# Kernel tuning notes

Hardware: AMD Instinct MI355X
Metric: run time of the kernel (lower is better)

The kernel has to match this reference:

```python
import jax, jax.numpy as jnp
import numpy as np

N, B, EMBED, ACT, DETER, STOCH, HID = 50, 256, 1536, 64, 2048, 64, 1024
EPS = 1e-3
MIN_STD, MAX_STD = 0.1, 2.0


def _p(key, shape, scale=0.02):
    return scale * jax.random.normal(key, shape, dtype=jnp.float32)


def setup_inputs() -> dict:
    key = jax.random.key(0)
    ks = jax.random.split(key, 20)
    inp = {
        "embed": jax.random.normal(ks[0], (N, B, EMBED), dtype=jnp.float32),
        "action": jax.random.normal(ks[1], (N, B, ACT), dtype=jnp.float32),
        "reset": jnp.zeros((N, B), dtype=bool),
        "h0": jnp.zeros((B, DETER), dtype=jnp.float32),
        "z0": jnp.zeros((B, STOCH), dtype=jnp.float32),
        "noises": jax.random.normal(ks[2], (N, B, STOCH), dtype=jnp.float32),
        # params
        "z_w": _p(ks[3], (STOCH, HID)), "z_b": jnp.zeros((HID,), jnp.float32),
        "a_w": _p(ks[4], (ACT, HID)),
        "in_g": jnp.ones((HID,), jnp.float32), "in_b": jnp.zeros((HID,), jnp.float32),
        "gru_wi": _p(ks[5], (HID, 3 * DETER)), "gru_wh": _p(ks[6], (DETER, 3 * DETER)),
        "gru_bi": jnp.zeros((3 * DETER,), jnp.float32), "gru_bh": jnp.zeros((3 * DETER,), jnp.float32),
        "ph_w": _p(ks[7], (DETER, HID)), "ph_b": jnp.zeros((HID,), jnp.float32),
        "pe_w": _p(ks[8], (EMBED, HID)),
        "pon_g": jnp.ones((HID,), jnp.float32), "pon_b": jnp.zeros((HID,), jnp.float32),
        "pom_w": _p(ks[9], (HID, 2 * STOCH)), "pom_b": jnp.zeros((2 * STOCH,), jnp.float32),
        "prh_w": _p(ks[10], (DETER, HID)), "prh_b": jnp.zeros((HID,), jnp.float32),
        "prn_g": jnp.ones((HID,), jnp.float32), "prn_b": jnp.zeros((HID,), jnp.float32),
        "prm_w": _p(ks[11], (HID, 2 * STOCH)), "prm_b": jnp.zeros((2 * STOCH,), jnp.float32),
    }
    return inp


def _ln(x, g, b):
    m = x.mean(-1, keepdims=True)
    v = ((x - m) ** 2).mean(-1, keepdims=True)
    return (x - m) * jax.lax.rsqrt(v + EPS) * g + b


def _rssm(embed, action, reset, h0, z0, noises,
          z_w, z_b, a_w, in_g, in_b, gru_wi, gru_wh, gru_bi, gru_bh,
          ph_w, ph_b, pe_w, pon_g, pon_b, pom_w, pom_b,
          prh_w, prh_b, prn_g, prn_b, prm_w, prm_b):
    mask = (~reset).astype(jnp.float32)[..., None]  # [n,b,1]

    def step(carry, xs):
        h, z = carry
        e, a, m, nz = xs
        h = h * m
        z = z * m
        x = z @ z_w + z_b + a @ a_w
        za = jax.nn.elu(_ln(x, in_g, in_b))
        gi = za @ gru_wi + gru_bi
        gh = h @ gru_wh + gru_bh
        ir, iu, ic = jnp.split(gi, 3, axis=-1)
        hr, hu, hc = jnp.split(gh, 3, axis=-1)
        r = jax.nn.sigmoid(ir + hr)
        u = jax.nn.sigmoid(iu + hu)
        c = jnp.tanh(ic + r * hc)
        h = (1.0 - u) * c + u * h
        x = h @ ph_w + ph_b + e @ pe_w
        post_in = jax.nn.elu(_ln(x, pon_g, pon_b))
        post = post_in @ pom_w + pom_b
        mean, raw = jnp.split(post, 2, axis=-1)
        std = MAX_STD * jax.nn.sigmoid(raw) + MIN_STD
        z = mean + std * nz
        return (h, z), (post, h, z)

    (_, _), (posts, hs, zs) = jax.lax.scan(step, (h0, z0), (embed, action, mask, noises))
    # batch prior over all states_h
    x = hs @ prh_w + prh_b
    priors = jax.nn.elu(_ln(x, prn_g, prn_b)) @ prm_w + prm_b
    features = jnp.concatenate([hs, zs], axis=-1)  # [n,b,deter+stoch]
    n, b = embed.shape[:2]
    out = jnp.concatenate([priors, posts, features], axis=-1)
    return out.reshape(n, b, 1, -1)  # I=1


def reference(embed, action, reset, h0, z0, noises,
              z_w, z_b, a_w, in_g, in_b, gru_wi, gru_wh, gru_bi, gru_bh,
              ph_w, ph_b, pe_w, pon_g, pon_b, pom_w, pom_b,
              prh_w, prh_b, prn_g, prn_b, prm_w, prm_b):
    return _rssm(embed, action, reset, h0, z0, noises,
                 z_w, z_b, a_w, in_g, in_b, gru_wi, gru_wh, gru_bi, gru_bh,
                 ph_w, ph_b, pe_w, pon_g, pon_b, pom_w, pom_b,
                 prh_w, prh_b, prn_g, prn_b, prm_w, prm_b)
```

## Files before the change

kernel.cpp:

```cpp
#include <hip/hip_runtime.h>
#include <hip/hip_bf16.h>

typedef __attribute__((ext_vector_type(8))) short short8;
typedef __attribute__((ext_vector_type(4))) short short4v;
typedef __attribute__((ext_vector_type(4))) float floatx4;

#define MFMA16x32(a, b, c) __builtin_amdgcn_mfma_f32_16x16x32_bf16((a), (b), (c), 0, 0, 0)
#define GLDS(gp, lp) __builtin_amdgcn_global_load_lds( \
    (__attribute__((address_space(1))) unsigned int*)(gp), \
    (__attribute__((address_space(3))) unsigned int*)(lp), 16, 0, 0)

#define NSTEP 50
#define BDIM  256
#define EMBD  1536
#define DETER 2048
#define STOCH 64
#define HID   1024
#define OUTW  2368
#define LNEPS 1e-3f

__device__ __forceinline__ unsigned short f2bf(float f) {
  union { float f; unsigned u; } v; v.f = f;
  unsigned r = v.u + 0x7fffu + ((v.u >> 16) & 1u);
  return (unsigned short)(r >> 16);
}
__device__ __forceinline__ float bf2f(unsigned short h) {
  union { unsigned u; float f; } v; v.u = (unsigned)h << 16;
  return v.f;
}
__device__ __forceinline__ float sgm(float x) { return 1.f / (1.f + __expf(-x)); }
__device__ __forceinline__ float elu1(float x) { return x > 0.f ? x : expm1f(x); }

__device__ __forceinline__ void block_sum2(float& s, float& q, float* red, int tid) {
  #pragma unroll
  for (int m = 1; m < 64; m <<= 1) { s += __shfl_xor(s, m, 64); q += __shfl_xor(q, m, 64); }
  int w = tid >> 6;
  if ((tid & 63) == 0) { red[w * 2] = s; red[w * 2 + 1] = q; }
  __syncthreads();
  s = red[0] + red[2] + red[4] + red[6];
  q = red[1] + red[3] + red[5] + red[7];
}

__global__ void k_transpose_bf16(const float* __restrict__ src, int N,
                                 unsigned short* __restrict__ dst, int ldd) {
  __shared__ float tile[32][33];
  int n0 = blockIdx.x * 32, k0 = blockIdx.y * 32;
  for (int i = threadIdx.y; i < 32; i += 8)
    tile[i][threadIdx.x] = src[(size_t)(k0 + i) * N + n0 + threadIdx.x];
  __syncthreads();
  for (int i = threadIdx.y; i < 32; i += 8)
    dst[(size_t)(n0 + i) * ldd + k0 + threadIdx.x] = f2bf(tile[threadIdx.x][i]);
}

__global__ void k_wt_gate(const float* __restrict__ wi, const float* __restrict__ wh,
                          unsigned short* __restrict__ dst) {
  __shared__ float tile[32][33];
  int r0 = blockIdx.x * 32, k0 = blockIdx.y * 32;
  int rr = r0 + threadIdx.x;
  int j = (rr / 48) * 16 + (rr & 15), g = (rr % 48) >> 4;
  int c = g * 2048 + j;
  for (int i = threadIdx.y; i < 32; i += 8) {
    int k = k0 + i;
    tile[i][threadIdx.x] = (k < 1024) ? wi[(size_t)k * 6144 + c]
                                      : wh[(size_t)(k - 1024) * 6144 + c];
  }
  __syncthreads();
  for (int i = threadIdx.y; i < 32; i += 8)
    dst[(size_t)(r0 + i) * 3072 + k0 + threadIdx.x] = f2bf(tile[threadIdx.x][i]);
}

__global__ void k_cvt_bf16(const float* __restrict__ src, unsigned short* __restrict__ dst, int n) {
  int i = blockIdx.x * blockDim.x + threadIdx.x;
  if (i < n) dst[i] = f2bf(src[i]);
}

__global__ void k_cvt4(const float* __restrict__ src, unsigned short* __restrict__ dst, int n4) {
  int i = blockIdx.x * 256 + threadIdx.x;
  if (i < n4) {
    floatx4 v = ((const floatx4*)src)[i];
    short4v o;
    #pragma unroll
    for (int j = 0; j < 4; j++) o[j] = (short)f2bf(v[j]);
    ((short4v*)dst)[i] = o;
  }
}

__global__ void k_init_state(const float* __restrict__ h0, const unsigned char* __restrict__ reset,
                             float* __restrict__ h_f32, unsigned short* __restrict__ hnb0) {
  int i = blockIdx.x * 256 + threadIdx.x;
  if (i < BDIM * DETER) {
    float m = reset[i >> 11] ? 0.f : 1.f;
    float v = h0[i] * m;
    h_f32[i] = v;
    hnb0[i] = f2bf(v);
  }
}

template <bool AF32, bool C16>
__global__ __launch_bounds__(256) void k_gemm(
    const void* __restrict__ Ap, long lda,
    const unsigned short* __restrict__ Bt, long ldb,
    const float* __restrict__ bias,
    void* __restrict__ Cp, long ldc, int K) {
  __shared__ __attribute__((aligned(16))) short A_s[64][72];
  __shared__ __attribute__((aligned(16))) short B_s[64][72];
  int n0 = blockIdx.x * 64, m0 = blockIdx.y * 64;
  int tid = threadIdx.x, wave = tid >> 6, lane = tid & 63;
  int srow = tid >> 3, skk = (tid & 7) * 8;
  int fr = lane & 15, fq = lane >> 4;
  int mb = (wave & 1) * 32, nb = (wave >> 1) * 32;
  const unsigned short* a16 = (const unsigned short*)Ap;
  const float* a32 = (const float*)Ap;
  floatx4 acc[2][2] = {};
  for (int k0 = 0; k0 < K; k0 += 64) {
    short8 av0, av1, bv0, bv1;
    if constexpr (AF32) {
      floatx4 f0 = *(const floatx4*)(a32 + (size_t)(m0 + srow) * lda + k0 + skk);
      floatx4 f1 = *(const floatx4*)(a32 + (size_t)(m0 + srow) * lda + k0 + skk + 4);
      floatx4 f2 = *(const floatx4*)(a32 + (size_t)(m0 + srow + 32) * lda + k0 + skk);
      floatx4 f3 = *(const floatx4*)(a32 + (size_t)(m0 + srow + 32) * lda + k0 + skk + 4);
      #pragma unroll
      for (int i = 0; i < 4; i++) {
        av0[i] = (short)f2bf(f0[i]); av0[4 + i] = (short)f2bf(f1[i]);
        av1[i] = (short)f2bf(f2[i]); av1[4 + i] = (short)f2bf(f3[i]);
      }
    } else {
      av0 = *(const short8*)(a16 + (size_t)(m0 + srow) * lda + k0 + skk);
      av1 = *(const short8*)(a16 + (size_t)(m0 + srow + 32) * lda + k0 + skk);
    }
    bv0 = *(const short8*)(Bt + (size_t)(n0 + srow) * ldb + k0 + skk);
    bv1 = *(const short8*)(Bt + (size_t)(n0 + srow + 32) * ldb + k0 + skk);
    __syncthreads();
    *(short8*)&A_s[srow][skk] = av0;
    *(short8*)&A_s[32 + srow][skk] = av1;
    *(short8*)&B_s[srow][skk] = bv0;
    *(short8*)&B_s[32 + srow][skk] = bv1;
    __syncthreads();
    #pragma unroll
    for (int ks = 0; ks < 2; ks++) {
      short8 a0 = *(const short8*)&A_s[mb + fr][ks * 32 + fq * 8];
      short8 a1 = *(const short8*)&A_s[mb + 16 + fr][ks * 32 + fq * 8];
      short8 b0 = *(const short8*)&B_s[nb + fr][ks * 32 + fq * 8];
      short8 b1 = *(const short8*)&B_s[nb + 16 + fr][ks * 32 + fq * 8];
      acc[0][0] = MFMA16x32(a0, b0, acc[0][0]);
      acc[0][1] = MFMA16x32(a0, b1, acc[0][1]);
      acc[1][0] = MFMA16x32(a1, b0, acc[1][0]);
      acc[1][1] = MFMA16x32(a1, b1, acc[1][1]);
    }
  }
  #pragma unroll
  for (int mi = 0; mi < 2; mi++)
    #pragma unroll
    for (int ni = 0; ni < 2; ni++)
      #pragma unroll
      for (int j = 0; j < 4; j++) {
        int row = m0 + mb + mi * 16 + fq * 4 + j;
        int col = n0 + nb + ni * 16 + fr;
        float v = acc[mi][ni][j];
        if (bias) v += bias[col];
        if constexpr (C16) ((unsigned short*)Cp)[(size_t)row * ldc + col] = f2bf(v);
        else               ((float*)Cp)[(size_t)row * ldc + col] = v;
      }
}

template <bool C16>
__global__ __launch_bounds__(256) void k_gemm2(
    const unsigned short* __restrict__ A, long lda,
    const unsigned short* __restrict__ Bt, long ldb,
    const float* __restrict__ bias,
    void* __restrict__ Cp, long ldc, int K) {
  __shared__ __attribute__((aligned(1024))) unsigned short lds[2][256 * 64];
  int per = gridDim.x >> 3;
  int flat = (blockIdx.x & 7) * per + (blockIdx.x >> 3);
  int n0 = (flat & 7) * 128, m0 = (flat >> 3) * 128;
  int tid = threadIdx.x, w = tid >> 6, lane = tid & 63;
  int lr = lane >> 3, ce = ((lane & 7) ^ lr) << 3;
  int fr = lane & 15, fq = lane >> 4;
  int xr = (fr & 7) << 3;
  int wm = (w & 1) * 64, wn = (w >> 1) * 64;
  auto stage = [&](int buf, int k0) {
    #pragma unroll
    for (int q = 0; q < 8; q++) {
      int j = w * 8 + q;
      int rr = j * 8 + lr;
      const unsigned short* src = (rr < 128)
        ? A + (size_t)(m0 + rr) * lda + k0 + ce
        : Bt + (size_t)(n0 + rr - 128) * ldb + k0 + ce;
      GLDS(src, &lds[buf][j * 512]);
    }
  };
  floatx4 acc[4][4] = {};
  int niter = K / 64;
  stage(0, 0); stage(1, 64);
  for (int ks = 0; ks < niter; ks++) {
    int cur = ks & 1;
    if (ks + 1 < niter) asm volatile("s_waitcnt vmcnt(8)" ::: "memory");
    else                asm volatile("s_waitcnt vmcnt(0)" ::: "memory");
    __builtin_amdgcn_s_barrier();
    __builtin_amdgcn_sched_barrier(0);
    const unsigned short* L = lds[cur];
    __builtin_amdgcn_s_setprio(1);
    #pragma unroll
    for (int kh = 0; kh < 2; kh++) {
      int kb = kh * 32 + fq * 8;
      short8 af[4], bf[4];
      #pragma unroll
      for (int i = 0; i < 4; i++) {
        af[i] = *(const short8*)&L[((wm + i * 16 + fr) * 64 + kb) ^ xr];
        bf[i] = *(const short8*)&L[((128 + wn + i * 16 + fr) * 64 + kb) ^ xr];
      }
      #pragma unroll
      for (int mi = 0; mi < 4; mi++)
        #pragma unroll
        for (int ni = 0; ni < 4; ni++)
          acc[mi][ni] = MFMA16x32(af[mi], bf[ni], acc[mi][ni]);
    }
    __builtin_amdgcn_s_setprio(0);
    __builtin_amdgcn_sched_barrier(0);
    __builtin_amdgcn_s_barrier();
    if (ks + 2 < niter) stage(cur, (ks + 2) * 64);
  }
  #pragma unroll
  for (int mi = 0; mi < 4; mi++)
    #pragma unroll
    for (int ni = 0; ni < 4; ni++)
      #pragma unroll
      for (int j = 0; j < 4; j++) {
        int row = m0 + wm + mi * 16 + fq * 4 + j;
        int col = n0 + wn + ni * 16 + fr;
        float v = acc[mi][ni][j];
        if (bias) v += bias[col];
        if constexpr (C16) ((unsigned short*)Cp)[(size_t)row * ldc + col] = f2bf(v);
        else               ((float*)Cp)[(size_t)row * ldc + col] = v;
      }
}

__global__ __launch_bounds__(512) void k_gru(
    int t, const unsigned short* __restrict__ astk, const unsigned short* __restrict__ hnb_r,
    const unsigned short* __restrict__ wt,
    const float* __restrict__ gbi, const float* __restrict__ gbh,
    const unsigned char* __restrict__ reset,
    float* __restrict__ h_f32, unsigned short* __restrict__ hnb_w,
    unsigned short* __restrict__ hs_bf, float* __restrict__ out) {
  __shared__ __attribute__((aligned(1024))) unsigned short lds[2][192 * 64];
  int raw = blockIdx.x;
  int xcd = raw & 7, ii = raw >> 3;
  int n_t = xcd * 8 + (ii & 7), m_t = ii >> 3;
  int m0 = m_t * 64;
  int tid = threadIdx.x, w = tid >> 6, lane = tid & 63;
  int lr = lane >> 3;
  int ce = ((lane & 7) ^ lr) << 3;
  int fr = lane & 15, fq = lane >> 4;
  int xr = (fr & 7) << 3;
  int wr = w & 1, wc = (w >> 1) & 1, kh = w >> 2;

  auto stage = [&](int buf, int k0) {
    #pragma unroll
    for (int q = 0; q < 3; q++) {
      int j = w * 3 + q;
      int rr = j * 8 + lr;
      const unsigned short* src;
      if (rr < 64) {
        src = (k0 < HID) ? astk + (size_t)(m0 + rr) * HID + (k0 + ce)
                         : hnb_r + (size_t)(m0 + rr) * DETER + (k0 - HID + ce);
      } else {
        int wrow = rr - 64;
        if (wrow > 95) wrow = 95;
        src = wt + (size_t)(n_t * 96 + wrow) * 3072 + (k0 + ce);
      }
      GLDS(src, &lds[buf][j * 512]);
    }
  };

  floatx4 acc[2][4] = {};
  stage(0, 0); stage(1, 64);
  for (int ks = 0; ks < 48; ks++) {
    int cur = ks & 1;
    if (ks < 47) asm volatile("s_waitcnt vmcnt(3)" ::: "memory");
    else         asm volatile("s_waitcnt vmcnt(0)" ::: "memory");
    __builtin_amdgcn_s_barrier();
    __builtin_amdgcn_sched_barrier(0);
    const unsigned short* L = lds[cur];
    __builtin_amdgcn_s_setprio(1);
    {
      int kb = kh * 32 + fq * 8;
      short8 a0 = *(const short8*)&L[((wr * 32 + fr) * 64 + kb) ^ xr];
      short8 a1 = *(const short8*)&L[((wr * 32 + 16 + fr) * 64 + kb) ^ xr];
      short8 br = *(const short8*)&L[((64 + wc * 48 + fr) * 64 + kb) ^ xr];
      short8 bu = *(const short8*)&L[((64 + wc * 48 + 16 + fr) * 64 + kb) ^ xr];
      short8 bc = *(const short8*)&L[((64 + wc * 48 + 32 + fr) * 64 + kb) ^ xr];
      acc[0][0] = MFMA16x32(a0, br, acc[0][0]);
      acc[1][0] = MFMA16x32(a1, br, acc[1][0]);
      acc[0][1] = MFMA16x32(a0, bu, acc[0][1]);
      acc[1][1] = MFMA16x32(a1, bu, acc[1][1]);
      if (ks < 16) {
        acc[0][2] = MFMA16x32(a0, bc, acc[0][2]);
        acc[1][2] = MFMA16x32(a1, bc, acc[1][2]);
      } else {
        acc[0][3] = MFMA16x32(a0, bc, acc[0][3]);
        acc[1][3] = MFMA16x32(a1, bc, acc[1][3]);
      }
    }
    __builtin_amdgcn_s_setprio(0);
    __builtin_amdgcn_sched_barrier(0);
    __builtin_amdgcn_s_barrier();
    if (ks + 2 < 48) stage(cur, (ks + 2) * 64);
  }
  __syncthreads();
  float* red = (float*)lds;
  if (w >= 4) {
    int base = ((w - 4) * 64 + lane) * 36;
    #pragma unroll
    for (int mi = 0; mi < 2; mi++)
      #pragma unroll
      for (int g = 0; g < 4; g++)
        *(floatx4*)&red[base + (mi * 4 + g) * 4] = acc[mi][g];
  }
  __syncthreads();
  if (w < 4) {
    int base = (w * 64 + lane) * 36;
    #pragma unroll
    for (int mi = 0; mi < 2; mi++)
      #pragma unroll
      for (int g = 0; g < 4; g++)
        acc[mi][g] += *(const floatx4*)&red[base + (mi * 4 + g) * 4];
    int jc = n_t * 32 + wc * 16 + fr;
    float bir = gbi[jc],        bhr = gbh[jc];
    float biu = gbi[jc + 2048], bhu = gbh[jc + 2048];
    float bic = gbi[jc + 4096], bhc = gbh[jc + 4096];
    #pragma unroll
    for (int mi = 0; mi < 2; mi++)
      #pragma unroll
      for (int j = 0; j < 4; j++) {
        int b = m0 + wr * 32 + mi * 16 + fq * 4 + j;
        float r = sgm(acc[mi][0][j] + bir + bhr);
        float u = sgm(acc[mi][1][j] + biu + bhu);
        float c = tanhf(acc[mi][2][j] + bic + r * (acc[mi][3][j] + bhc));
        size_t hi = (size_t)b * DETER + jc;
        float hold = h_f32[hi];
        float hn = (1.f - u) * c + u * hold;
        out[((size_t)t * BDIM + b) * OUTW + 256 + jc] = hn;
        hs_bf[((size_t)t * BDIM + b) * DETER + jc] = f2bf(hn);
        float mn = (t + 1 < NSTEP && reset[(size_t)(t + 1) * BDIM + b]) ? 0.f : 1.f;
        float hm = hn * mn;
        h_f32[hi] = hm;
        hnb_w[hi] = f2bf(hm);
      }
  }
}

__global__ __launch_bounds__(256) void k_ph(
    int t, const unsigned short* __restrict__ hsbf, const unsigned short* __restrict__ pht,
    float* __restrict__ x2p) {
  __shared__ __attribute__((aligned(1024))) unsigned short lds[2][96 * 64];
  int raw = blockIdx.x;
  int n_t = raw & 15, m_t = (raw >> 4) & 7, kslc = raw >> 7;
  int m0 = m_t * 32, n0 = n_t * 64, koff = kslc * 1024;
  const unsigned short* hb = hsbf + (size_t)t * BDIM * DETER;
  int tid = threadIdx.x, w = tid >> 6, lane = tid & 63;
  int lr = lane >> 3;
  int ce = ((lane & 7) ^ lr) << 3;
  int fr = lane & 15, fq = lane >> 4;
  int xr = (fr & 7) << 3;

  auto stage = [&](int buf, int k0) {
    #pragma unroll
    for (int q = 0; q < 3; q++) {
      int j = w * 3 + q;
      int rr = j * 8 + lr;
      const unsigned short* src = (rr < 32)
          ? hb + (size_t)(m0 + rr) * DETER + koff + k0 + ce
          : pht + (size_t)(n0 + rr - 32) * DETER + koff + k0 + ce;
      GLDS(src, &lds[buf][j * 512]);
    }
  };

  floatx4 acc[2] = {};
  stage(0, 0); stage(1, 64);
  for (int ks = 0; ks < 16; ks++) {
    int cur = ks & 1;
    if (ks < 15) asm volatile("s_waitcnt vmcnt(3)" ::: "memory");
    else         asm volatile("s_waitcnt vmcnt(0)" ::: "memory");
    __builtin_amdgcn_s_barrier();
    __builtin_amdgcn_sched_barrier(0);
    const unsigned short* L = lds[cur];
    __builtin_amdgcn_s_setprio(1);
    #pragma unroll
    for (int kh = 0; kh < 2; kh++) {
      int kb = kh * 32 + fq * 8;
      short8 a0 = *(const short8*)&L[((fr) * 64 + kb) ^ xr];
      short8 a1 = *(const short8*)&L[((16 + fr) * 64 + kb) ^ xr];
      short8 bw = *(const short8*)&L[((32 + w * 16 + fr) * 64 + kb) ^ xr];
      acc[0] = MFMA16x32(a0, bw, acc[0]);
      acc[1] = MFMA16x32(a1, bw, acc[1]);
    }
    __builtin_amdgcn_s_setprio(0);
    __builtin_amdgcn_sched_barrier(0);
    __builtin_amdgcn_s_barrier();
    if (ks + 2 < 16) stage(cur, (ks + 2) * 64);
  }
  int col = n0 + w * 16 + fr;
  #pragma unroll
  for (int mi = 0; mi < 2; mi++)
    #pragma unroll
    for (int j = 0; j < 4; j++)
      x2p[(size_t)(kslc * BDIM + m0 + mi * 16 + fq * 4 + j) * HID + col] = acc[mi][j];
}

__global__ __launch_bounds__(256) void k_post(
    int t, const float* __restrict__ x2p, const float* __restrict__ ph_b,
    const unsigned short* __restrict__ eab,
    const float* __restrict__ pon_g, const float* __restrict__ pon_b,
    const unsigned short* __restrict__ pomb, const float* __restrict__ pom_b,
    const float* __restrict__ noises, const unsigned char* __restrict__ reset,
    const unsigned short* __restrict__ zwb, const unsigned short* __restrict__ xab,
    const float* __restrict__ in_g, const float* __restrict__ in_b,
    float* __restrict__ out, unsigned short* __restrict__ astk) {
  int b = blockIdx.x, tid = threadIdx.x;
  __shared__ float pin[HID];
  __shared__ float red[8];
  __shared__ float post[128];
  __shared__ float zm[64];
  __shared__ float pacc[256];
  int j0 = tid * 4;
  floatx4 x = *(const floatx4*)&x2p[(size_t)b * HID + j0];
  floatx4 x1 = *(const floatx4*)&x2p[(size_t)(BDIM + b) * HID + j0];
  floatx4 bb = *(const floatx4*)&ph_b[j0];
  short4v e4 = *(const short4v*)&eab[((size_t)t * BDIM + b) * HID + j0];
  #pragma unroll
  for (int i = 0; i < 4; i++) x[i] += x1[i] + bb[i] + bf2f((unsigned short)e4[i]);
  float s = x[0] + x[1] + x[2] + x[3];
  float q = x[0]*x[0] + x[1]*x[1] + x[2]*x[2] + x[3]*x[3];
  block_sum2(s, q, red, tid);
  float mean = s * (1.f / HID);
  float rstd = rsqrtf(q * (1.f / HID) - mean * mean + LNEPS);
  floatx4 gg = *(const floatx4*)&pon_g[j0];
  floatx4 ob = *(const floatx4*)&pon_b[j0];
  floatx4 pv;
  #pragma unroll
  for (int i = 0; i < 4; i++) pv[i] = elu1((x[i] - mean) * rstd * gg[i] + ob[i]);
  *(floatx4*)&pin[j0] = pv;
  __syncthreads();
  {
    int col = tid & 127, half = tid >> 7;
    const unsigned short* pb = pomb + (size_t)(half * 512) * 128 + col;
    const float* pi = pin + half * 512;
    float a0 = 0, a1 = 0, a2 = 0, a3 = 0;
    #pragma unroll 8
    for (int k = 0; k < 512; k += 4) {
      a0 += pi[k]     * bf2f(pb[(size_t)k * 128]);
      a1 += pi[k + 1] * bf2f(pb[(size_t)(k + 1) * 128]);
      a2 += pi[k + 2] * bf2f(pb[(size_t)(k + 2) * 128]);
      a3 += pi[k + 3] * bf2f(pb[(size_t)(k + 3) * 128]);
    }
    pacc[tid] = (a0 + a1) + (a2 + a3);
  }
  __syncthreads();
  size_t ro = ((size_t)t * BDIM + b) * OUTW;
  if (tid < 128) {
    float p = pacc[tid] + pacc[tid + 128] + pom_b[tid];
    post[tid] = p;
    out[ro + 128 + tid] = p;
  }
  __syncthreads();
  if (tid < 64) {
    float mn = post[tid], raw = post[64 + tid];
    float std = 2.f * sgm(raw) + 0.1f;
    float z = mn + std * noises[((size_t)t * BDIM + b) * STOCH + tid];
    out[ro + 2304 + tid] = z;
    float mk = (t + 1 < NSTEP && reset[(size_t)(t + 1) * BDIM + b]) ? 0.f : 1.f;
    zm[tid] = z * mk;
  }
  __syncthreads();
  if (t + 1 < NSTEP) {
    short4v xa = *(const short4v*)&xab[((size_t)(t + 1) * BDIM + b) * HID + j0];
    floatx4 xn;
    #pragma unroll
    for (int i = 0; i < 4; i++) xn[i] = bf2f((unsigned short)xa[i]);
    #pragma unroll 8
    for (int k = 0; k < 64; k++) {
      short4v wv4 = *(const short4v*)&zwb[(size_t)k * HID + j0];
      float zk = zm[k];
      #pragma unroll
      for (int i = 0; i < 4; i++) xn[i] += zk * bf2f((unsigned short)wv4[i]);
    }
    float s2 = xn[0] + xn[1] + xn[2] + xn[3];
    float q2 = xn[0]*xn[0] + xn[1]*xn[1] + xn[2]*xn[2] + xn[3]*xn[3];
    block_sum2(s2, q2, red, tid);
    float mean2 = s2 * (1.f / HID);
    float rstd2 = rsqrtf(q2 * (1.f / HID) - mean2 * mean2 + LNEPS);
    floatx4 g2 = *(const floatx4*)&in_g[j0];
    floatx4 b2 = *(const floatx4*)&in_b[j0];
    short4v ov;
    #pragma unroll
    for (int i = 0; i < 4; i++)
      ov[i] = (short)f2bf(elu1((xn[i] - mean2) * rstd2 * g2[i] + b2[i]));
    *(short4v*)&astk[(size_t)b * HID + j0] = ov;
  }
}

__global__ __launch_bounds__(256) void k_pre0(
    const float* __restrict__ z0, const unsigned char* __restrict__ reset,
    const float* __restrict__ z_w, const unsigned short* __restrict__ xab,
    const float* __restrict__ in_g, const float* __restrict__ in_b,
    unsigned short* __restrict__ astk) {
  int b = blockIdx.x, tid = threadIdx.x;
  __shared__ float zm[64];
  __shared__ float red[8];
  if (tid < 64) {
    float mk = reset[b] ? 0.f : 1.f;
    zm[tid] = z0[(size_t)b * STOCH + tid] * mk;
  }
  __syncthreads();
  int j0 = tid * 4;
  short4v xa = *(const short4v*)&xab[(size_t)b * HID + j0];
  floatx4 xn;
  #pragma unroll
  for (int i = 0; i < 4; i++) xn[i] = bf2f((unsigned short)xa[i]);
  #pragma unroll 8
  for (int k = 0; k < 64; k++) {
    floatx4 wv = *(const floatx4*)&z_w[(size_t)k * HID + j0];
    xn += zm[k] * wv;
  }
  float s = xn[0] + xn[1] + xn[2] + xn[3];
  float q = xn[0]*xn[0] + xn[1]*xn[1] + xn[2]*xn[2] + xn[3]*xn[3];
  block_sum2(s, q, red, tid);
  float mean = s * (1.f / HID);
  float rstd = rsqrtf(q * (1.f / HID) - mean * mean + LNEPS);
  short4v ov;
  #pragma unroll
  for (int i = 0; i < 4; i++)
    ov[i] = (short)f2bf(elu1((xn[i] - mean) * rstd * in_g[j0 + i] + in_b[j0 + i]));
  *(short4v*)&astk[(size_t)b * HID + j0] = ov;
}

__global__ __launch_bounds__(256) void k_ln_elu(
    const unsigned short* __restrict__ X, const float* __restrict__ g, const float* __restrict__ bb,
    unsigned short* __restrict__ Y) {
  int row = blockIdx.x, tid = threadIdx.x;
  __shared__ float red[8];
  int j0 = tid * 4;
  short4v v4 = *(const short4v*)&X[(size_t)row * HID + j0];
  floatx4 v;
  #pragma unroll
  for (int i = 0; i < 4; i++) v[i] = bf2f((unsigned short)v4[i]);
  float s = v[0] + v[1] + v[2] + v[3];
  float q = v[0]*v[0] + v[1]*v[1] + v[2]*v[2] + v[3]*v[3];
  block_sum2(s, q, red, tid);
  float mean = s * (1.f / HID);
  float rstd = rsqrtf(q * (1.f / HID) - mean * mean + LNEPS);
  short4v ov;
  #pragma unroll
  for (int i = 0; i < 4; i++)
    ov[i] = (short)f2bf(elu1((v[i] - mean) * rstd * g[j0 + i] + bb[j0 + i]));
  *(short4v*)&Y[(size_t)row * HID + j0] = ov;
}

extern "C" void kernel_launch(void* const* d_in, const int* in_sizes, int n_in,
                              void* d_out, int out_size, void* d_ws, size_t ws_size,
                              hipStream_t stream) {
  (void)in_sizes; (void)n_in; (void)out_size; (void)ws_size;
  const float* embed  = (const float*)d_in[0];
  const float* action = (const float*)d_in[1];
  const unsigned char* reset = (const unsigned char*)d_in[2];
  const float* h0     = (const float*)d_in[3];
  const float* z0     = (const float*)d_in[4];
  const float* noises = (const float*)d_in[5];
  const float* z_w    = (const float*)d_in[6];
  const float* z_b    = (const float*)d_in[7];
  const float* a_w    = (const float*)d_in[8];
  const float* in_g   = (const float*)d_in[9];
  const float* in_b   = (const float*)d_in[10];
  const float* gru_wi = (const float*)d_in[11];
  const float* gru_wh = (const float*)d_in[12];
  const float* gru_bi = (const float*)d_in[13];
  const float* gru_bh = (const float*)d_in[14];
  const float* ph_w   = (const float*)d_in[15];
  const float* ph_b   = (const float*)d_in[16];
  const float* pe_w   = (const float*)d_in[17];
  const float* pon_g  = (const float*)d_in[18];
  const float* pon_b  = (const float*)d_in[19];
  const float* pom_w  = (const float*)d_in[20];
  const float* pom_b  = (const float*)d_in[21];
  const float* prh_w  = (const float*)d_in[22];
  const float* prh_b  = (const float*)d_in[23];
  const float* prn_g  = (const float*)d_in[24];
  const float* prn_b  = (const float*)d_in[25];
  const float* prm_w  = (const float*)d_in[26];
  const float* prm_b  = (const float*)d_in[27];
  float* out = (float*)d_out;

  char* w = (char*)d_ws;
  auto carve = [&](size_t bytes) { char* p = w; w += (bytes + 255) & ~(size_t)255; return p; };
  unsigned short* WT   = (unsigned short*)carve((size_t)6144 * 3072 * 2);
  unsigned short* PHT  = (unsigned short*)carve((size_t)HID * DETER * 2);
  unsigned short* PET  = (unsigned short*)carve((size_t)HID * EMBD * 2);
  unsigned short* AWT  = (unsigned short*)carve((size_t)HID * 64 * 2);
  unsigned short* ZWB  = (unsigned short*)carve((size_t)STOCH * HID * 2);
  unsigned short* POMB = (unsigned short*)carve((size_t)HID * 128 * 2);
  unsigned short* PRHT = (unsigned short*)carve((size_t)HID * DETER * 2);
  unsigned short* PRMT = (unsigned short*)carve((size_t)128 * HID * 2);
  unsigned short* EAB  = (unsigned short*)carve((size_t)NSTEP * BDIM * HID * 2);
  unsigned short* XPB  = (unsigned short*)carve((size_t)NSTEP * BDIM * HID * 2);
  unsigned short* XABP = (unsigned short*)carve((size_t)NSTEP * BDIM * HID * 2);
  unsigned short* HSBF = (unsigned short*)carve((size_t)NSTEP * BDIM * DETER * 2);
  unsigned short* ASTK = (unsigned short*)carve((size_t)BDIM * HID * 2);
  unsigned short* HNB0 = (unsigned short*)carve((size_t)BDIM * DETER * 2);
  unsigned short* HNB1 = (unsigned short*)carve((size_t)BDIM * DETER * 2);
  float*          HF32 = (float*)carve((size_t)BDIM * DETER * 4);
  float*          X2P  = (float*)carve((size_t)2 * BDIM * HID * 4);
  unsigned short* EMBB = HSBF;

  dim3 tb(32, 8);
  k_wt_gate<<<dim3(192, 96), tb, 0, stream>>>(gru_wi, gru_wh, WT);
  k_transpose_bf16<<<dim3(32, 64), tb, 0, stream>>>(ph_w, 1024, PHT, DETER);
  k_transpose_bf16<<<dim3(32, 48), tb, 0, stream>>>(pe_w, 1024, PET, EMBD);
  k_transpose_bf16<<<dim3(32, 2), tb, 0, stream>>>(a_w, 1024, AWT, 64);
  k_transpose_bf16<<<dim3(32, 64), tb, 0, stream>>>(prh_w, 1024, PRHT, DETER);
  k_transpose_bf16<<<dim3(4, 32), tb, 0, stream>>>(prm_w, 128, PRMT, HID);
  k_cvt_bf16<<<512, 256, 0, stream>>>(pom_w, POMB, HID * 128);
  k_cvt_bf16<<<256, 256, 0, stream>>>(z_w, ZWB, STOCH * HID);
  k_init_state<<<2048, 256, 0, stream>>>(h0, reset, HF32, HNB0);
  k_cvt4<<<(NSTEP * BDIM * EMBD / 4 + 255) / 256, 256, 0, stream>>>(embed, EMBB, NSTEP * BDIM * EMBD / 4);
  k_gemm<true, true><<<dim3(16, 200), 256, 0, stream>>>(action, 64, AWT, 64, z_b, XABP, HID, 64);
  k_gemm2<true><<<800, 256, 0, stream>>>(EMBB, EMBD, PET, EMBD, nullptr, EAB, HID, EMBD);
  k_pre0<<<BDIM, 256, 0, stream>>>(z0, reset, z_w, XABP, in_g, in_b, ASTK);

  for (int t = 0; t < NSTEP; t++) {
    const unsigned short* hr = (t & 1) ? HNB1 : HNB0;
    unsigned short* hw = (t & 1) ? HNB0 : HNB1;
    k_gru<<<256, 512, 0, stream>>>(t, ASTK, hr, WT, gru_bi, gru_bh, reset,
                                   HF32, hw, HSBF, out);
    k_ph<<<256, 256, 0, stream>>>(t, HSBF, PHT, X2P);
    k_post<<<BDIM, 256, 0, stream>>>(t, X2P, ph_b, EAB, pon_g, pon_b, POMB, pom_b,
                                     noises, reset, ZWB, XABP, in_g, in_b, out, ASTK);
  }

  k_gemm2<true><<<800, 256, 0, stream>>>(HSBF, DETER, PRHT, DETER, prh_b, XPB, HID, DETER);
  k_ln_elu<<<NSTEP * BDIM, 256, 0, stream>>>(XPB, prn_g, prn_b, XABP);
  k_gemm<false, false><<<dim3(2, 200), 256, 0, stream>>>(XABP, HID, PRMT, HID, prm_b, out, OUTW, HID);
}
```

Measured before the change: 2.838 ms.

## Split K-halves across extra waves in gemm2 and ph kernels with LDS reduction

Doubles the block size of k_gemm2 and k_ph to 512 threads. Each group of four waves now handles one 32-wide half of every 64-wide K slice instead of one wave looping over both halves, and the two partial accumulators are summed through LDS before the store. The goal is more waves in flight to hide latency, particularly in the small per-step k_ph launched 50 times. The cost is an extra LDS reduction with two block barriers, higher register/occupancy pressure for gemm2's 64-accumulator tiles, and redundant clamped B-row loads in k_ph.

```diff
diff --git a/kernel.cpp b/kernel.cpp
--- a/kernel.cpp
+++ b/kernel.cpp
@@ -164,7 +164,7 @@
 }
 
 template <bool C16>
-__global__ __launch_bounds__(256) void k_gemm2(
+__global__ __launch_bounds__(512) void k_gemm2(
     const unsigned short* __restrict__ A, long lda,
     const unsigned short* __restrict__ Bt, long ldb,
     const float* __restrict__ bias,
@@ -177,11 +177,11 @@
   int lr = lane >> 3, ce = ((lane & 7) ^ lr) << 3;
   int fr = lane & 15, fq = lane >> 4;
   int xr = (fr & 7) << 3;
-  int wm = (w & 1) * 64, wn = (w >> 1) * 64;
+  int wm = (w & 1) * 64, wn = ((w >> 1) & 1) * 64, kh = w >> 2;
   auto stage = [&](int buf, int k0) {
     #pragma unroll
-    for (int q = 0; q < 8; q++) {
-      int j = w * 8 + q;
+    for (int q = 0; q < 4; q++) {
+      int j = w * 4 + q;
       int rr = j * 8 + lr;
       const unsigned short* src = (rr < 128)
         ? A + (size_t)(m0 + rr) * lda + k0 + ce
@@ -194,14 +194,13 @@
   stage(0, 0); stage(1, 64);
   for (int ks = 0; ks < niter; ks++) {
     int cur = ks & 1;
-    if (ks + 1 < niter) asm volatile("s_waitcnt vmcnt(8)" ::: "memory");
+    if (ks + 1 < niter) asm volatile("s_waitcnt vmcnt(4)" ::: "memory");
     else                asm volatile("s_waitcnt vmcnt(0)" ::: "memory");
     __builtin_amdgcn_s_barrier();
     __builtin_amdgcn_sched_barrier(0);
     const unsigned short* L = lds[cur];
     __builtin_amdgcn_s_setprio(1);
-    #pragma unroll
-    for (int kh = 0; kh < 2; kh++) {
+    {
       int kb = kh * 32 + fq * 8;
       short8 af[4], bf[4];
       #pragma unroll
@@ -220,19 +219,42 @@
     __builtin_amdgcn_s_barrier();
     if (ks + 2 < niter) stage(cur, (ks + 2) * 64);
   }
-  #pragma unroll
-  for (int mi = 0; mi < 4; mi++)
-    #pragma unroll
-    for (int ni = 0; ni < 4; ni++)
-      #pragma unroll
-      for (int j = 0; j < 4; j++) {
-        int row = m0 + wm + mi * 16 + fq * 4 + j;
-        int col = n0 + wn + ni * 16 + fr;
-        float v = acc[mi][ni][j];
-        if (bias) v += bias[col];
-        if constexpr (C16) ((unsigned short*)Cp)[(size_t)row * ldc + col] = f2bf(v);
-        else               ((float*)Cp)[(size_t)row * ldc + col] = v;
-      }
+  __syncthreads();
+  float* red = (float*)lds;
+  if (kh == 1) {
+    int p = w - 4;
+    #pragma unroll
+    for (int mi = 0; mi < 4; mi++)
+      #pragma unroll
+      for (int ni = 0; ni < 4; ni++) {
+        int g = mi * 4 + ni;
+        *(floatx4*)&red[((g * 4 + p) * 64 + lane) * 4] = acc[mi][ni];
+      }
+  }
+  __syncthreads();
+  if (kh == 0) {
+    int p = w;
+    #pragma unroll
+    for (int mi = 0; mi < 4; mi++)
+      #pragma unroll
+      for (int ni = 0; ni < 4; ni++) {
+        int g = mi * 4 + ni;
+        acc[mi][ni] += *(const floatx4*)&red[((g * 4 + p) * 64 + lane) * 4];
+      }
+    #pragma unroll
+    for (int mi = 0; mi < 4; mi++)
+      #pragma unroll
+      for (int ni = 0; ni < 4; ni++)
+        #pragma unroll
+        for (int j = 0; j < 4; j++) {
+          int row = m0 + wm + mi * 16 + fq * 4 + j;
+          int col = n0 + wn + ni * 16 + fr;
+          float v = acc[mi][ni][j];
+          if (bias) v += bias[col];
+          if constexpr (C16) ((unsigned short*)Cp)[(size_t)row * ldc + col] = f2bf(v);
+          else               ((float*)Cp)[(size_t)row * ldc + col] = v;
+        }
+  }
 }
 
 __global__ __launch_bounds__(512) void k_gru(
@@ -349,10 +371,10 @@
   }
 }
 
-__global__ __launch_bounds__(256) void k_ph(
+__global__ __launch_bounds__(512) void k_ph(
     int t, const unsigned short* __restrict__ hsbf, const unsigned short* __restrict__ pht,
     float* __restrict__ x2p) {
-  __shared__ __attribute__((aligned(1024))) unsigned short lds[2][96 * 64];
+  __shared__ __attribute__((aligned(1024))) unsigned short lds[2][128 * 64];
   int raw = blockIdx.x;
   int n_t = raw & 15, m_t = (raw >> 4) & 7, kslc = raw >> 7;
   int m0 = m_t * 32, n0 = n_t * 64, koff = kslc * 1024;
@@ -362,15 +384,21 @@
   int ce = ((lane & 7) ^ lr) << 3;
   int fr = lane & 15, fq = lane >> 4;
   int xr = (fr & 7) << 3;
+  int wc = w & 3, kh = w >> 2;
 
   auto stage = [&](int buf, int k0) {
     #pragma unroll
-    for (int q = 0; q < 3; q++) {
-      int j = w * 3 + q;
+    for (int q = 0; q < 2; q++) {
+      int j = w * 2 + q;
       int rr = j * 8 + lr;
-      const unsigned short* src = (rr < 32)
-          ? hb + (size_t)(m0 + rr) * DETER + koff + k0 + ce
-          : pht + (size_t)(n0 + rr - 32) * DETER + koff + k0 + ce;
+      const unsigned short* src;
+      if (rr < 32) {
+        src = hb + (size_t)(m0 + rr) * DETER + koff + k0 + ce;
+      } else {
+        int brow = rr - 32;
+        if (brow > 63) brow = 63;
+        src = pht + (size_t)(n0 + brow) * DETER + koff + k0 + ce;
+      }
       GLDS(src, &lds[buf][j * 512]);
     }
   };
@@ -379,18 +407,17 @@
   stage(0, 0); stage(1, 64);
   for (int ks = 0; ks < 16; ks++) {
     int cur = ks & 1;
-    if (ks < 15) asm volatile("s_waitcnt vmcnt(3)" ::: "memory");
+    if (ks < 15) asm volatile("s_waitcnt vmcnt(2)" ::: "memory");
     else         asm volatile("s_waitcnt vmcnt(0)" ::: "memory");
     __builtin_amdgcn_s_barrier();
     __builtin_amdgcn_sched_barrier(0);
     const unsigned short* L = lds[cur];
     __builtin_amdgcn_s_setprio(1);
-    #pragma unroll
-    for (int kh = 0; kh < 2; kh++) {
+    {
       int kb = kh * 32 + fq * 8;
       short8 a0 = *(const short8*)&L[((fr) * 64 + kb) ^ xr];
       short8 a1 = *(const short8*)&L[((16 + fr) * 64 + kb) ^ xr];
-      short8 bw = *(const short8*)&L[((32 + w * 16 + fr) * 64 + kb) ^ xr];
+      short8 bw = *(const short8*)&L[((32 + wc * 16 + fr) * 64 + kb) ^ xr];
       acc[0] = MFMA16x32(a0, bw, acc[0]);
       acc[1] = MFMA16x32(a1, bw, acc[1]);
     }
@@ -399,12 +426,27 @@
     __builtin_amdgcn_s_barrier();
     if (ks + 2 < 16) stage(cur, (ks + 2) * 64);
   }
-  int col = n0 + w * 16 + fr;
-  #pragma unroll
-  for (int mi = 0; mi < 2; mi++)
-    #pragma unroll
-    for (int j = 0; j < 4; j++)
-      x2p[(size_t)(kslc * BDIM + m0 + mi * 16 + fq * 4 + j) * HID + col] = acc[mi][j];
+  __syncthreads();
+  float* red = (float*)lds;
+  if (kh == 1) {
+    int p = w - 4;
+    #pragma unroll
+    for (int g = 0; g < 2; g++)
+      *(floatx4*)&red[((g * 4 + p) * 64 + lane) * 4] = acc[g];
+  }
+  __syncthreads();
+  if (kh == 0) {
+    int p = w;
+    #pragma unroll
+    for (int g = 0; g < 2; g++)
+      acc[g] += *(const floatx4*)&red[((g * 4 + p) * 64 + lane) * 4];
+    int col = n0 + wc * 16 + fr;
+    #pragma unroll
+    for (int mi = 0; mi < 2; mi++)
+      #pragma unroll
+      for (int j = 0; j < 4; j++)
+        x2p[(size_t)(kslc * BDIM + m0 + mi * 16 + fq * 4 + j) * HID + col] = acc[mi][j];
+  }
 }
 
 __global__ __launch_bounds__(256) void k_post(
@@ -623,7 +665,7 @@
   k_init_state<<<2048, 256, 0, stream>>>(h0, reset, HF32, HNB0);
   k_cvt4<<<(NSTEP * BDIM * EMBD / 4 + 255) / 256, 256, 0, stream>>>(embed, EMBB, NSTEP * BDIM * EMBD / 4);
   k_gemm<true, true><<<dim3(16, 200), 256, 0, stream>>>(action, 64, AWT, 64, z_b, XABP, HID, 64);
-  k_gemm2<true><<<800, 256, 0, stream>>>(EMBB, EMBD, PET, EMBD, nullptr, EAB, HID, EMBD);
+  k_gemm2<true><<<800, 512, 0, stream>>>(EMBB, EMBD, PET, EMBD, nullptr, EAB, HID, EMBD);
   k_pre0<<<BDIM, 256, 0, stream>>>(z0, reset, z_w, XABP, in_g, in_b, ASTK);
 
   for (int t = 0; t < NSTEP; t++) {
@@ -631,12 +673,12 @@
     unsigned short* hw = (t & 1) ? HNB0 : HNB1;
     k_gru<<<256, 512, 0, stream>>>(t, ASTK, hr, WT, gru_bi, gru_bh, reset,
                                    HF32, hw, HSBF, out);
-    k_ph<<<256, 256, 0, stream>>>(t, HSBF, PHT, X2P);
+    k_ph<<<256, 512, 0, stream>>>(t, HSBF, PHT, X2P);
     k_post<<<BDIM, 256, 0, stream>>>(t, X2P, ph_b, EAB, pon_g, pon_b, POMB, pom_b,
                                      noises, reset, ZWB, XABP, in_g, in_b, out, ASTK);
   }
 
-  k_gemm2<true><<<800, 256, 0, stream>>>(HSBF, DETER, PRHT, DETER, prh_b, XPB, HID, DETER);
+  k_gemm2<true><<<800, 512, 0, stream>>>(HSBF, DETER, PRHT, DETER, prh_b, XPB, HID, DETER);
   k_ln_elu<<<NSTEP * BDIM, 256, 0, stream>>>(XPB, prn_g, prn_b, XABP);
   k_gemm<false, false><<<dim3(2, 200), 256, 0, stream>>>(XABP, HID, PRMT, HID, prm_b, out, OUTW, HID);
 }
```

Result: no change. 2.878 ms (+1.4%).
